# Kernel optimization log

Measured on AMD Instinct MI355X. Metric: run time of the kernel, lower is better.

Reference implementation:

```python
import jax, jax.numpy as jnp
import numpy as np

N_NODES = 100000
N_EDGES = 3200000
N_GRAPHS = 256
HID = 128


def _glorot(key, shape):
    fan_in = shape[1]
    return jax.random.normal(key, shape, dtype=jnp.float32) / jnp.sqrt(jnp.float32(fan_in))


def setup_inputs() -> dict:
    key = jax.random.key(0)
    ks = jax.random.split(key, 16)
    x = jax.random.normal(ks[0], (N_NODES, 50), dtype=jnp.float32)
    edge_index = jax.random.randint(ks[1], (2, N_EDGES), 0, N_NODES, dtype=jnp.int32)
    batch = jnp.sort(jax.random.randint(ks[2], (N_NODES,), 0, N_GRAPHS, dtype=jnp.int32))
    d1, d2, d3 = HID, HID * 2, HID * 4
    params = {
        'w1l': _glorot(ks[3], (d1, 50)), 'b1': jnp.zeros((d1,), jnp.float32), 'w1r': _glorot(ks[4], (d1, 50)),
        'w2l': _glorot(ks[5], (d2, d1)), 'b2': jnp.zeros((d2,), jnp.float32), 'w2r': _glorot(ks[6], (d2, d1)),
        'w3l': _glorot(ks[7], (d3, d2)), 'b3': jnp.zeros((d3,), jnp.float32), 'w3r': _glorot(ks[8], (d3, d2)),
        'fc1_w': _glorot(ks[9], (d2, d3)), 'fc1_b': jnp.zeros((d2,), jnp.float32),
        'fc2_w': _glorot(ks[10], (d1, d2)), 'fc2_b': jnp.zeros((d1,), jnp.float32),
        'cls_w': _glorot(ks[11], (15, d1)), 'cls_b': jnp.zeros((15,), jnp.float32),
    }
    return {'x': x, 'edge_index': edge_index, 'batch': batch, **params}


def _sage_conv(x, src, dst, wl, b, wr):
    # PyG SAGEConv (mean aggr): out = lin_l(mean_j x_j) + lin_r(x_i)
    agg = jax.ops.segment_sum(x[src], dst, num_segments=N_NODES)
    deg = jax.ops.segment_sum(jnp.ones((src.shape[0],), x.dtype), dst, num_segments=N_NODES)
    agg = agg / jnp.maximum(deg, 1.0)[:, None]
    return agg @ wl.T + b + x @ wr.T


def reference(x, edge_index, batch,
              w1l, b1, w1r, w2l, b2, w2r, w3l, b3, w3r,
              fc1_w, fc1_b, fc2_w, fc2_b, cls_w, cls_b):
    src, dst = edge_index[0], edge_index[1]
    # eval mode: dropout is identity
    h = jax.nn.leaky_relu(_sage_conv(x, src, dst, w1l, b1, w1r), negative_slope=0.01)
    h = jax.nn.relu(_sage_conv(h, src, dst, w2l, b2, w2r))
    h = jax.nn.relu(_sage_conv(h, src, dst, w3l, b3, w3r))
    # global mean pool over graphs
    pooled = jax.ops.segment_sum(h, batch, num_segments=N_GRAPHS)
    cnt = jax.ops.segment_sum(jnp.ones((h.shape[0],), h.dtype), batch, num_segments=N_GRAPHS)
    pooled = pooled / jnp.maximum(cnt, 1.0)[:, None]
    z = jax.nn.relu(pooled @ fc1_w.T + fc1_b)
    z = jax.nn.relu(z @ fc2_w.T + fc2_b)
    return z @ cls_w.T + cls_b
```

## Files before the change

### kernel.cpp

```cpp
#include <hip/hip_runtime.h>
#include <hip/hip_bf16.h>

#define N_NODES 100000
#define N_EDGES 3200000
#define N_GRAPHS 256
#define CAP 80
#define NB 1563
#define NPB 64
#define PBLK 512
#define EPB 6250

typedef __hip_bfloat16 bf16;
using f32x4  = __attribute__((ext_vector_type(4))) float;
using f32x2  = __attribute__((ext_vector_type(2))) float;
using short8 = __attribute__((ext_vector_type(8))) short;

__global__ __launch_bounds__(256) void p1_count(const int* __restrict__ dst,
                                                int* __restrict__ bcount) {
    __shared__ int hist[NB];
    int i = blockIdx.x;
    for (int b = threadIdx.x; b < NB; b += 256) hist[b] = 0;
    __syncthreads();
    int base = i * EPB;
    for (int j = threadIdx.x; j < EPB; j += 256)
        atomicAdd(&hist[dst[base + j] >> 6], 1);
    __syncthreads();
    for (int b = threadIdx.x; b < NB; b += 256) bcount[(size_t)b * PBLK + i] = hist[b];
}

__global__ __launch_bounds__(512) void p2a_total(const int* __restrict__ bcount,
                                                 int* __restrict__ btotal) {
    __shared__ int red[512];
    int b = blockIdx.x;
    red[threadIdx.x] = bcount[(size_t)b * PBLK + threadIdx.x];
    __syncthreads();
    for (int off = 256; off > 0; off >>= 1) {
        if (threadIdx.x < off) red[threadIdx.x] += red[threadIdx.x + off];
        __syncthreads();
    }
    if (threadIdx.x == 0) btotal[b] = red[0];
}

__global__ __launch_bounds__(1024) void p2b_scan(const int* __restrict__ btotal,
                                                 int* __restrict__ bbase) {
    __shared__ int buf[1024];
    __shared__ int carry;
    if (threadIdx.x == 0) carry = 0;
    __syncthreads();
    for (int t = 0; t < NB; t += 1024) {
        int i = t + threadIdx.x;
        int v = (i < NB) ? btotal[i] : 0;
        buf[threadIdx.x] = v;
        __syncthreads();
        for (int off = 1; off < 1024; off <<= 1) {
            int tv = (threadIdx.x >= off) ? buf[threadIdx.x - off] : 0;
            __syncthreads();
            buf[threadIdx.x] += tv;
            __syncthreads();
        }
        if (i < NB) bbase[i] = carry + buf[threadIdx.x] - v;
        __syncthreads();
        if (threadIdx.x == 0) carry += buf[1023];
        __syncthreads();
    }
    if (threadIdx.x == 0) bbase[NB] = carry;
}

__global__ __launch_bounds__(512) void p2c_off(const int* __restrict__ bcount,
                                               const int* __restrict__ bbase,
                                               int* __restrict__ off) {
    __shared__ int buf[512];
    int b = blockIdx.x;
    int v = bcount[(size_t)b * PBLK + threadIdx.x];
    buf[threadIdx.x] = v;
    __syncthreads();
    for (int o = 1; o < 512; o <<= 1) {
        int t = (threadIdx.x >= o) ? buf[threadIdx.x - o] : 0;
        __syncthreads();
        buf[threadIdx.x] += t;
        __syncthreads();
    }
    off[(size_t)threadIdx.x * NB + b] = bbase[b] + buf[threadIdx.x] - v;
}

__global__ __launch_bounds__(256) void p3_scatter(const int* __restrict__ src,
                                                  const int* __restrict__ dst,
                                                  const int* __restrict__ off,
                                                  unsigned int* __restrict__ ebuf) {
    __shared__ int loff[NB];
    int i = blockIdx.x;
    for (int b = threadIdx.x; b < NB; b += 256) loff[b] = off[(size_t)i * NB + b];
    __syncthreads();
    int base = i * EPB;
    for (int j = threadIdx.x; j < EPB; j += 256) {
        int d = dst[base + j];
        int p = atomicAdd(&loff[d >> 6], 1);
        ebuf[p] = ((unsigned)src[base + j] << 6) | (unsigned)(d & 63);
    }
}

__global__ __launch_bounds__(256) void p4_csr(const unsigned int* __restrict__ ebuf,
                                              const int* __restrict__ bbase,
                                              int* __restrict__ cols, int* __restrict__ cnt,
                                              float* __restrict__ invdeg) {
    __shared__ int lcnt[NPB];
    int b = blockIdx.x;
    if (threadIdx.x < NPB) lcnt[threadIdx.x] = 0;
    __syncthreads();
    int s = bbase[b], e = bbase[b + 1];
    int n0 = b * NPB;
    for (int j = s + threadIdx.x; j < e; j += 256) {
        unsigned int p = ebuf[j];
        int dl = p & 63;
        int r = atomicAdd(&lcnt[dl], 1);
        if (r < CAP) cols[(size_t)(n0 + dl) * CAP + r] = (int)(p >> 6);
    }
    __syncthreads();
    if (threadIdx.x < NPB) {
        int n = n0 + threadIdx.x;
        if (n < N_NODES) {
            int c = lcnt[threadIdx.x];
            cnt[n] = c;
            invdeg[n] = 1.0f / fmaxf((float)c, 1.0f);
        }
    }
}

__global__ void xprep_kernel(const float* __restrict__ x, unsigned char* __restrict__ xb8) {
    int t = blockIdx.x * blockDim.x + threadIdx.x;
    if (t >= N_NODES * 64) return;
    int n = t >> 6, f = t & 63;
    float v = (f < 50) ? x[(size_t)n * 50 + f] : 0.f;
    int p = __builtin_amdgcn_cvt_pk_fp8_f32(v, v, 0, false);
    xb8[t] = (unsigned char)(p & 0xff);
}

__device__ __forceinline__ void wcvt(const float* __restrict__ s, bf16* __restrict__ d,
                                     int Din, int Kp, int lt) {
    int o = lt / Kp, kk = lt % Kp;
    d[lt] = __float2bfloat16(kk < Din ? s[(size_t)o * Din + kk] : 0.f);
}

__global__ void wprep_all_kernel(const float* w1l, const float* w1r,
                                 const float* w2l, const float* w2r,
                                 const float* w3l, const float* w3r,
                                 bf16* w1l_b, bf16* w1r_b, bf16* w2l_b, bf16* w2r_b,
                                 bf16* w3l_b, bf16* w3r_b) {
    int t = blockIdx.x * blockDim.x + threadIdx.x;
    if      (t < 8192)   wcvt(w1l, w1l_b, 50, 64, t);
    else if (t < 16384)  wcvt(w1r, w1r_b, 50, 64, t - 8192);
    else if (t < 49152)  wcvt(w2l, w2l_b, 128, 128, t - 16384);
    else if (t < 81920)  wcvt(w2r, w2r_b, 128, 128, t - 49152);
    else if (t < 212992) wcvt(w3l, w3l_b, 256, 256, t - 81920);
    else if (t < 344064) wcvt(w3r, w3r_b, 256, 256, t - 212992);
}

template <int D>
__global__ void aggv8_kernel(const unsigned char* __restrict__ h8,
                             const int* __restrict__ cnt,
                             const int* __restrict__ cols, const float* __restrict__ invdeg,
                             unsigned char* __restrict__ AG8) {
    constexpr int L = D / 8;
    int n = blockIdx.x * (256 / L) + threadIdx.x / L;
    int lane = threadIdx.x % L;
    if (n >= N_NODES) return;
    const int* cp = cols + (size_t)n * CAP;
    int deg = min(cnt[n], CAP);
    float acc[8] = {};
    auto accum = [&](uint2 v) {
        f32x2 a0 = __builtin_amdgcn_cvt_pk_f32_fp8(v.x, false);
        f32x2 a1 = __builtin_amdgcn_cvt_pk_f32_fp8(v.x, true);
        f32x2 a2 = __builtin_amdgcn_cvt_pk_f32_fp8(v.y, false);
        f32x2 a3 = __builtin_amdgcn_cvt_pk_f32_fp8(v.y, true);
        acc[0] += a0[0]; acc[1] += a0[1]; acc[2] += a1[0]; acc[3] += a1[1];
        acc[4] += a2[0]; acc[5] += a2[1]; acc[6] += a3[0]; acc[7] += a3[1];
    };
    int j = 0;
    for (; j + 8 <= deg; j += 8) {
        uint2 v[8];
#pragma unroll
        for (int q = 0; q < 8; ++q)
            v[q] = *(const uint2*)&h8[(size_t)cp[j + q] * D + lane * 8];
#pragma unroll
        for (int q = 0; q < 8; ++q) accum(v[q]);
    }
    for (; j < deg; ++j) accum(*(const uint2*)&h8[(size_t)cp[j] * D + lane * 8]);
    float inv = invdeg[n];
    uint2 o;
    int w0 = __builtin_amdgcn_cvt_pk_fp8_f32(acc[0] * inv, acc[1] * inv, 0, false);
    w0     = __builtin_amdgcn_cvt_pk_fp8_f32(acc[2] * inv, acc[3] * inv, w0, true);
    int w1 = __builtin_amdgcn_cvt_pk_fp8_f32(acc[4] * inv, acc[5] * inv, 0, false);
    w1     = __builtin_amdgcn_cvt_pk_fp8_f32(acc[6] * inv, acc[7] * inv, w1, true);
    o.x = (unsigned)w0; o.y = (unsigned)w1;
    *(uint2*)&AG8[(size_t)n * D + lane * 8] = o;
}

__device__ __forceinline__ short8 cvt8(uint2 v) {
    f32x2 p0 = __builtin_amdgcn_cvt_pk_f32_fp8(v.x, false);
    f32x2 p1 = __builtin_amdgcn_cvt_pk_f32_fp8(v.x, true);
    f32x2 p2 = __builtin_amdgcn_cvt_pk_f32_fp8(v.y, false);
    f32x2 p3 = __builtin_amdgcn_cvt_pk_f32_fp8(v.y, true);
    union { short8 s; bf16 h[8]; } r;
    r.h[0] = __float2bfloat16(p0[0]); r.h[1] = __float2bfloat16(p0[1]);
    r.h[2] = __float2bfloat16(p1[0]); r.h[3] = __float2bfloat16(p1[1]);
    r.h[4] = __float2bfloat16(p2[0]); r.h[5] = __float2bfloat16(p2[1]);
    r.h[6] = __float2bfloat16(p3[0]); r.h[7] = __float2bfloat16(p3[1]);
    return r.s;
}

template <int ACT, int POOL, int NX>
__global__ __launch_bounds__(256) void fp8a_gemm(
        const unsigned char* __restrict__ A1, const unsigned char* __restrict__ A2, int Kh,
        const bf16* __restrict__ B1, const bf16* __restrict__ B2,
        const float* __restrict__ bias, unsigned char* __restrict__ out8,
        int M, int Dout,
        const int* __restrict__ batch, float* __restrict__ pooled) {
    __shared__ alignas(16) bf16 As[2][128][32];
    __shared__ alignas(16) bf16 Bs[2][128][32];
    __shared__ int sbatch[128];

    const int gid = blockIdx.x;
    const int group = gid / (8 * NX);
    const int rem = gid % (8 * NX);
    const int xcol = rem >> 3;
    const int ytile = group * 8 + (rem & 7);
    const int MBt = (M + 127) >> 7;
    if (ytile >= MBt) return;

    const int tid = threadIdx.x;
    const int n0 = ytile * 128;
    const int o0 = xcol * 128;

    if (POOL && tid < 128) {
        int n = n0 + tid;
        sbatch[tid] = (n < M) ? batch[n] : -1;
    }

    const int lane = tid & 63;
    const int w = tid >> 6;
    const int wr = w >> 1, wc = w & 1;
    const int lr = lane & 15, hi = lane >> 4;
    const int l4 = lane >> 2;
    const int kc8 = (lane & 3) * 8;

    f32x4 acc[4][4] = {};

    const int rl0 = w * 32 + l4;
    const int rl1 = rl0 + 16;

    auto issueA = [&](int k0, uint2& a0, uint2& a1v) {
        const unsigned char* Ap = (k0 < Kh) ? A1 : A2;
        int kk = (k0 < Kh) ? k0 : k0 - Kh;
        a0  = *(const uint2*)&Ap[(size_t)min(n0 + rl0, M - 1) * Kh + kk + kc8];
        a1v = *(const uint2*)&Ap[(size_t)min(n0 + rl1, M - 1) * Kh + kk + kc8];
    };
    auto issueB = [&](int buf, int k0) {
        const bf16* Bp = (k0 < Kh) ? B1 : B2;
        int kk = (k0 < Kh) ? k0 : k0 - Kh;
#pragma unroll
        for (int c = 0; c < 2; ++c) {
            int rl = w * 32 + c * 16 + l4;
            size_t gb = (size_t)(o0 + rl) * (size_t)Kh + kk + kc8;
            __builtin_amdgcn_global_load_lds(
                (const __attribute__((address_space(1))) void*)(Bp + gb),
                (__attribute__((address_space(3))) void*)&Bs[buf][w * 32 + c * 16][0], 16, 0, 0);
        }
    };
    auto writeA = [&](int buf, uint2 a0, uint2 a1v) {
        *(short8*)&As[buf][rl0][kc8] = cvt8(a0);
        *(short8*)&As[buf][rl1][kc8] = cvt8(a1v);
    };

    const int nt = (2 * Kh) / 32;
    uint2 ra0, ra1;
    issueA(0, ra0, ra1);
    issueB(0, 0);
    asm volatile("s_waitcnt vmcnt(0)" ::: "memory");
    writeA(0, ra0, ra1);
    __syncthreads();

    int cur = 0;
    for (int t = 0; t < nt; ++t) {
        if (t + 1 < nt) {
            issueA((t + 1) * 32, ra0, ra1);
            issueB(cur ^ 1, (t + 1) * 32);
        }

        short8 af[4], bfr[4];
#pragma unroll
        for (int m = 0; m < 4; ++m)
            af[m] = *(const short8*)&As[cur][wr * 64 + m * 16 + lr][hi * 8];
#pragma unroll
        for (int n = 0; n < 4; ++n)
            bfr[n] = *(const short8*)&Bs[cur][wc * 64 + n * 16 + lr][hi * 8];
#pragma unroll
        for (int m = 0; m < 4; ++m)
#pragma unroll
            for (int n = 0; n < 4; ++n)
                acc[m][n] = __builtin_amdgcn_mfma_f32_16x16x32_bf16(af[m], bfr[n], acc[m][n], 0, 0, 0);

        if (t + 1 < nt) {
            asm volatile("s_waitcnt vmcnt(0)" ::: "memory");
            writeA(cur ^ 1, ra0, ra1);
            __syncthreads();
        }
        cur ^= 1;
    }

    float bias_v[4];
#pragma unroll
    for (int n = 0; n < 4; ++n) bias_v[n] = bias[o0 + wc * 64 + n * 16 + lr];

    if (!POOL) {
#pragma unroll
        for (int m = 0; m < 4; ++m) {
#pragma unroll
            for (int j = 0; j < 4; ++j) {
                int row = n0 + wr * 64 + m * 16 + hi * 4 + j;
                if (row < M) {
#pragma unroll
                    for (int n = 0; n < 4; ++n) {
                        int col = o0 + wc * 64 + n * 16 + lr;
                        float s = acc[m][n][j] + bias_v[n];
                        if (ACT == 0) s = (s >= 0.f) ? s : 0.01f * s;
                        else          s = fmaxf(s, 0.f);
                        int p = __builtin_amdgcn_cvt_pk_fp8_f32(s, s, 0, false);
                        out8[(size_t)row * Dout + col] = (unsigned char)(p & 0xff);
                    }
                }
            }
        }
    } else {
        int lastv = min(127, M - 1 - n0);
        int gmin = sbatch[0], gmax = sbatch[lastv];
        for (int g = gmin; g <= gmax; ++g) {
            float s[4] = {0.f, 0.f, 0.f, 0.f};
#pragma unroll
            for (int m = 0; m < 4; ++m) {
#pragma unroll
                for (int j = 0; j < 4; ++j) {
                    int rl = wr * 64 + m * 16 + hi * 4 + j;
                    if (sbatch[rl] == g) {
#pragma unroll
                        for (int n = 0; n < 4; ++n)
                            s[n] += fmaxf(acc[m][n][j] + bias_v[n], 0.f);
                    }
                }
            }
#pragma unroll
            for (int n = 0; n < 4; ++n) {
                float v = s[n];
                v += __shfl_xor(v, 16, 64);
                v += __shfl_xor(v, 32, 64);
                if (hi == 0)
                    atomicAdd(&pooled[(size_t)g * 512 + o0 + wc * 64 + n * 16 + lr], v);
            }
        }
    }
}

__global__ void bounds_kernel(const int* __restrict__ batch, int* __restrict__ gstart) {
    int g = blockIdx.x * blockDim.x + threadIdx.x;
    if (g > N_GRAPHS) return;
    int lo = 0, hi = N_NODES;
    while (lo < hi) {
        int mid = (lo + hi) >> 1;
        if (batch[mid] < g) lo = mid + 1;
        else hi = mid;
    }
    gstart[g] = lo;
}

__global__ void pool_finalize(float* __restrict__ pooled, const int* __restrict__ gstart) {
    int g = blockIdx.x;
    int f = threadIdx.x;
    float cnt = fmaxf((float)(gstart[g + 1] - gstart[g]), 1.0f);
    pooled[(size_t)g * 512 + f] /= cnt;
}

template <int ACT>
__global__ void mlp_kernel(const float* __restrict__ in, const float* __restrict__ w,
                           const float* __restrict__ b, float* __restrict__ out,
                           int M, int K, int O) {
    int t = blockIdx.x * blockDim.x + threadIdx.x;
    if (t >= M * O) return;
    int m = t / O, o = t % O;
    const float* ip = in + (size_t)m * K;
    const float* wp = w + (size_t)o * K;
    float s = 0.f;
    for (int k = 0; k < K; ++k) s += ip[k] * wp[k];
    s += b[o];
    if (ACT) s = fmaxf(s, 0.f);
    out[(size_t)m * O + o] = s;
}

extern "C" void kernel_launch(void* const* d_in, const int* in_sizes, int n_in,
                              void* d_out, int out_size, void* d_ws, size_t ws_size,
                              hipStream_t stream) {
    const float* x     = (const float*)d_in[0];
    const int*   ei    = (const int*)d_in[1];
    const int*   batch = (const int*)d_in[2];
    const float* w1l = (const float*)d_in[3];
    const float* b1  = (const float*)d_in[4];
    const float* w1r = (const float*)d_in[5];
    const float* w2l = (const float*)d_in[6];
    const float* b2  = (const float*)d_in[7];
    const float* w2r = (const float*)d_in[8];
    const float* w3l = (const float*)d_in[9];
    const float* b3  = (const float*)d_in[10];
    const float* w3r = (const float*)d_in[11];
    const float* fc1_w = (const float*)d_in[12];
    const float* fc1_b = (const float*)d_in[13];
    const float* fc2_w = (const float*)d_in[14];
    const float* fc2_b = (const float*)d_in[15];
    const float* cls_w = (const float*)d_in[16];
    const float* cls_b = (const float*)d_in[17];
    float* out = (float*)d_out;

    const int* src = ei;
    const int* dst = ei + N_EDGES;

    char* wsp = (char*)d_ws;
    size_t used = 0;
    auto alloc = [&](size_t bytes) {
        char* p = wsp + used;
        used += (bytes + 255) & ~(size_t)255;
        return p;
    };
    int*   cnt    = (int*)alloc((size_t)N_NODES * 4);
    int*   cols   = (int*)alloc((size_t)N_NODES * CAP * 4);
    float* invdeg = (float*)alloc((size_t)N_NODES * 4);
    int*   gstart = (int*)alloc((size_t)(N_GRAPHS + 1) * 4);
    char*  xbdead = alloc((size_t)N_NODES * 64 * 2);
    char*  R      = alloc((size_t)N_NODES * 256 * 2);
    unsigned char* AG8 = (unsigned char*)R;
    char*  S51    = alloc((size_t)N_NODES * 256 * 2);
    unsigned char* h1_8 = (unsigned char*)alloc((size_t)N_NODES * 128);
    unsigned char* h2_8 = (unsigned char*)alloc((size_t)N_NODES * 256);
    bf16*  w1l_b  = (bf16*)alloc(128 * 64 * 2);
    bf16*  w1r_b  = (bf16*)alloc(128 * 64 * 2);
    bf16*  w2l_b  = (bf16*)alloc(256 * 128 * 2);
    bf16*  w2r_b  = (bf16*)alloc(256 * 128 * 2);
    bf16*  w3l_b  = (bf16*)alloc(512 * 256 * 2);
    bf16*  w3r_b  = (bf16*)alloc(512 * 256 * 2);
    float* pooled = (float*)alloc((size_t)N_GRAPHS * 512 * 4);
    float* z1     = (float*)alloc((size_t)N_GRAPHS * 256 * 4);
    float* z2     = (float*)alloc((size_t)N_GRAPHS * 128 * 4);
    (void)xbdead;

    int* bcount = (int*)(S51 + 16 * 1024 * 1024);
    int* btotal = bcount + (size_t)NB * PBLK;
    int* bbase  = btotal + NB;
    int* off    = bbase + NB + 1;
    unsigned int* ebuf = (unsigned int*)S51;
    unsigned char* xb8 = (unsigned char*)S51;

    if (ws_size < used) return;

    p1_count<<<PBLK, 256, 0, stream>>>(dst, bcount);
    p2a_total<<<NB, 512, 0, stream>>>(bcount, btotal);
    p2b_scan<<<1, 1024, 0, stream>>>(btotal, bbase);
    p2c_off<<<NB, 512, 0, stream>>>(bcount, bbase, off);
    p3_scatter<<<PBLK, 256, 0, stream>>>(src, dst, off, ebuf);
    p4_csr<<<NB, 256, 0, stream>>>(ebuf, bbase, cols, cnt, invdeg);
    bounds_kernel<<<2, 160, 0, stream>>>(batch, gstart);

    xprep_kernel<<<(N_NODES * 64 + 255) / 256, 256, 0, stream>>>(x, xb8);
    wprep_all_kernel<<<(344064 + 255) / 256, 256, 0, stream>>>(
        w1l, w1r, w2l, w2r, w3l, w3r, w1l_b, w1r_b, w2l_b, w2r_b, w3l_b, w3r_b);

    const int GB = 98 * 8;

    aggv8_kernel<64><<<(N_NODES * 8 + 255) / 256, 256, 0, stream>>>(
        xb8, cnt, cols, invdeg, AG8);
    fp8a_gemm<0, 0, 1><<<GB, 256, 0, stream>>>(
        AG8, xb8, 64, w1l_b, w1r_b, b1, h1_8, N_NODES, 128, nullptr, nullptr);

    aggv8_kernel<128><<<(N_NODES * 16 + 255) / 256, 256, 0, stream>>>(
        h1_8, cnt, cols, invdeg, AG8);
    fp8a_gemm<1, 0, 2><<<GB * 2, 256, 0, stream>>>(
        AG8, h1_8, 128, w2l_b, w2r_b, b2, h2_8, N_NODES, 256, nullptr, nullptr);

    aggv8_kernel<256><<<(N_NODES * 32 + 255) / 256, 256, 0, stream>>>(
        h2_8, cnt, cols, invdeg, AG8);
    hipMemsetAsync(pooled, 0, (size_t)N_GRAPHS * 512 * 4, stream);
    fp8a_gemm<1, 1, 4><<<GB * 4, 256, 0, stream>>>(
        AG8, h2_8, 256, w3l_b, w3r_b, b3, nullptr, N_NODES, 512, batch, pooled);
    pool_finalize<<<N_GRAPHS, 512, 0, stream>>>(pooled, gstart);

    mlp_kernel<1><<<(N_GRAPHS * 256 + 255) / 256, 256, 0, stream>>>(
        pooled, fc1_w, fc1_b, z1, N_GRAPHS, 512, 256);
    mlp_kernel<1><<<(N_GRAPHS * 128 + 255) / 256, 256, 0, stream>>>(
        z1, fc2_w, fc2_b, z2, N_GRAPHS, 256, 128);
    mlp_kernel<0><<<(N_GRAPHS * 15 + 255) / 256, 256, 0, stream>>>(
        z2, cls_w, cls_b, out, N_GRAPHS, 128, 15);
}
```

Before: 570.5 us.

## Switch GEMMs to native FP8 MFMA with hi/lo split FP8 weights

The GEMM kernels previously read FP8 activations, converted them to bf16 in registers and wrote them to LDS before running bf16 MFMA. Activations are now copied straight to LDS as FP8 with global_load_lds, and each weight is stored as a high FP8 part plus an FP8 residual, so fp8×fp8 MFMAs run twice per tile to keep weight precision. This removes the per-tile conversion work and the register-staged A path, and halves the LDS footprint of A. In exchange it doubles the MFMA count and adds the lo-weight loads, and accuracy relies on the residual split.

```diff
diff --git a/kernel.cpp b/kernel.cpp
--- a/kernel.cpp
+++ b/kernel.cpp
@@ -13,7 +13,6 @@
 typedef __hip_bfloat16 bf16;
 using f32x4  = __attribute__((ext_vector_type(4))) float;
 using f32x2  = __attribute__((ext_vector_type(2))) float;
-using short8 = __attribute__((ext_vector_type(8))) short;
 
 __global__ __launch_bounds__(256) void p1_count(const int* __restrict__ dst,
                                                 int* __restrict__ bcount) {
@@ -135,24 +134,32 @@
     xb8[t] = (unsigned char)(p & 0xff);
 }
 
-__device__ __forceinline__ void wcvt(const float* __restrict__ s, bf16* __restrict__ d,
-                                     int Din, int Kp, int lt) {
+__device__ __forceinline__ void wcvt2(const float* __restrict__ s, unsigned char* __restrict__ d,
+                                      int Din, int Kp, int Dout, int lt) {
     int o = lt / Kp, kk = lt % Kp;
-    d[lt] = __float2bfloat16(kk < Din ? s[(size_t)o * Din + kk] : 0.f);
+    float v = (kk < Din) ? s[(size_t)o * Din + kk] : 0.f;
+    int ph = __builtin_amdgcn_cvt_pk_fp8_f32(v, v, 0, false);
+    unsigned hb = (unsigned)(ph & 0xff);
+    f32x2 dec = __builtin_amdgcn_cvt_pk_f32_fp8(hb, false);
+    float r = v - dec[0];
+    int pl = __builtin_amdgcn_cvt_pk_fp8_f32(r, r, 0, false);
+    d[lt] = (unsigned char)hb;
+    d[(size_t)Dout * Kp + lt] = (unsigned char)(pl & 0xff);
 }
 
 __global__ void wprep_all_kernel(const float* w1l, const float* w1r,
                                  const float* w2l, const float* w2r,
                                  const float* w3l, const float* w3r,
-                                 bf16* w1l_b, bf16* w1r_b, bf16* w2l_b, bf16* w2r_b,
-                                 bf16* w3l_b, bf16* w3r_b) {
+                                 unsigned char* w1l_8, unsigned char* w1r_8,
+                                 unsigned char* w2l_8, unsigned char* w2r_8,
+                                 unsigned char* w3l_8, unsigned char* w3r_8) {
     int t = blockIdx.x * blockDim.x + threadIdx.x;
-    if      (t < 8192)   wcvt(w1l, w1l_b, 50, 64, t);
-    else if (t < 16384)  wcvt(w1r, w1r_b, 50, 64, t - 8192);
-    else if (t < 49152)  wcvt(w2l, w2l_b, 128, 128, t - 16384);
-    else if (t < 81920)  wcvt(w2r, w2r_b, 128, 128, t - 49152);
-    else if (t < 212992) wcvt(w3l, w3l_b, 256, 256, t - 81920);
-    else if (t < 344064) wcvt(w3r, w3r_b, 256, 256, t - 212992);
+    if      (t < 8192)   wcvt2(w1l, w1l_8, 50, 64, 128, t);
+    else if (t < 16384)  wcvt2(w1r, w1r_8, 50, 64, 128, t - 8192);
+    else if (t < 49152)  wcvt2(w2l, w2l_8, 128, 128, 256, t - 16384);
+    else if (t < 81920)  wcvt2(w2r, w2r_8, 128, 128, 256, t - 49152);
+    else if (t < 212992) wcvt2(w3l, w3l_8, 256, 256, 512, t - 81920);
+    else if (t < 344064) wcvt2(w3r, w3r_8, 256, 256, 512, t - 212992);
 }
 
 template <int D>
@@ -166,6 +173,7 @@
     if (n >= N_NODES) return;
     const int* cp = cols + (size_t)n * CAP;
     int deg = min(cnt[n], CAP);
+    const size_t fo = (size_t)lane * 8;
     float acc[8] = {};
     auto accum = [&](uint2 v) {
         f32x2 a0 = __builtin_amdgcn_cvt_pk_f32_fp8(v.x, false);
@@ -180,11 +188,11 @@
         uint2 v[8];
 #pragma unroll
         for (int q = 0; q < 8; ++q)
-            v[q] = *(const uint2*)&h8[(size_t)cp[j + q] * D + lane * 8];
+            v[q] = *(const uint2*)&h8[(size_t)cp[j + q] * D + fo];
 #pragma unroll
         for (int q = 0; q < 8; ++q) accum(v[q]);
     }
-    for (; j < deg; ++j) accum(*(const uint2*)&h8[(size_t)cp[j] * D + lane * 8]);
+    for (; j < deg; ++j) accum(*(const uint2*)&h8[(size_t)cp[j] * D + fo]);
     float inv = invdeg[n];
     uint2 o;
     int w0 = __builtin_amdgcn_cvt_pk_fp8_f32(acc[0] * inv, acc[1] * inv, 0, false);
@@ -192,31 +200,20 @@
     int w1 = __builtin_amdgcn_cvt_pk_fp8_f32(acc[4] * inv, acc[5] * inv, 0, false);
     w1     = __builtin_amdgcn_cvt_pk_fp8_f32(acc[6] * inv, acc[7] * inv, w1, true);
     o.x = (unsigned)w0; o.y = (unsigned)w1;
-    *(uint2*)&AG8[(size_t)n * D + lane * 8] = o;
-}
-
-__device__ __forceinline__ short8 cvt8(uint2 v) {
-    f32x2 p0 = __builtin_amdgcn_cvt_pk_f32_fp8(v.x, false);
-    f32x2 p1 = __builtin_amdgcn_cvt_pk_f32_fp8(v.x, true);
-    f32x2 p2 = __builtin_amdgcn_cvt_pk_f32_fp8(v.y, false);
-    f32x2 p3 = __builtin_amdgcn_cvt_pk_f32_fp8(v.y, true);
-    union { short8 s; bf16 h[8]; } r;
-    r.h[0] = __float2bfloat16(p0[0]); r.h[1] = __float2bfloat16(p0[1]);
-    r.h[2] = __float2bfloat16(p1[0]); r.h[3] = __float2bfloat16(p1[1]);
-    r.h[4] = __float2bfloat16(p2[0]); r.h[5] = __float2bfloat16(p2[1]);
-    r.h[6] = __float2bfloat16(p3[0]); r.h[7] = __float2bfloat16(p3[1]);
-    return r.s;
+    *(uint2*)&AG8[(size_t)n * D + fo] = o;
 }
 
 template <int ACT, int POOL, int NX>
-__global__ __launch_bounds__(256) void fp8a_gemm(
+__global__ __launch_bounds__(256) void fp8_gemm(
         const unsigned char* __restrict__ A1, const unsigned char* __restrict__ A2, int Kh,
-        const bf16* __restrict__ B1, const bf16* __restrict__ B2,
+        const unsigned char* __restrict__ B1h, const unsigned char* __restrict__ B1l,
+        const unsigned char* __restrict__ B2h, const unsigned char* __restrict__ B2l,
         const float* __restrict__ bias, unsigned char* __restrict__ out8,
         int M, int Dout,
         const int* __restrict__ batch, float* __restrict__ pooled) {
-    __shared__ alignas(16) bf16 As[2][128][32];
-    __shared__ alignas(16) bf16 Bs[2][128][32];
+    __shared__ alignas(16) unsigned char As[2][128][32];
+    __shared__ alignas(16) unsigned char Bsh[2][128][32];
+    __shared__ alignas(16) unsigned char Bsl[2][128][32];
     __shared__ int sbatch[128];
 
     const int gid = blockIdx.x;
@@ -240,70 +237,55 @@
     const int w = tid >> 6;
     const int wr = w >> 1, wc = w & 1;
     const int lr = lane & 15, hi = lane >> 4;
-    const int l4 = lane >> 2;
-    const int kc8 = (lane & 3) * 8;
+    const int srow = w * 32 + (lane >> 1);
+    const int scol = (lane & 1) * 16;
 
     f32x4 acc[4][4] = {};
 
-    const int rl0 = w * 32 + l4;
-    const int rl1 = rl0 + 16;
-
-    auto issueA = [&](int k0, uint2& a0, uint2& a1v) {
+    auto stage = [&](int buf, int k0) {
         const unsigned char* Ap = (k0 < Kh) ? A1 : A2;
+        const unsigned char* Bph = (k0 < Kh) ? B1h : B2h;
+        const unsigned char* Bpl = (k0 < Kh) ? B1l : B2l;
         int kk = (k0 < Kh) ? k0 : k0 - Kh;
-        a0  = *(const uint2*)&Ap[(size_t)min(n0 + rl0, M - 1) * Kh + kk + kc8];
-        a1v = *(const uint2*)&Ap[(size_t)min(n0 + rl1, M - 1) * Kh + kk + kc8];
+        size_t ga = (size_t)min(n0 + srow, M - 1) * (size_t)Kh + kk + scol;
+        __builtin_amdgcn_global_load_lds(
+            (const __attribute__((address_space(1))) void*)(Ap + ga),
+            (__attribute__((address_space(3))) void*)&As[buf][w * 32][0], 16, 0, 0);
+        size_t gb = (size_t)(o0 + srow) * (size_t)Kh + kk + scol;
+        __builtin_amdgcn_global_load_lds(
+            (const __attribute__((address_space(1))) void*)(Bph + gb),
+            (__attribute__((address_space(3))) void*)&Bsh[buf][w * 32][0], 16, 0, 0);
+        __builtin_amdgcn_global_load_lds(
+            (const __attribute__((address_space(1))) void*)(Bpl + gb),
+            (__attribute__((address_space(3))) void*)&Bsl[buf][w * 32][0], 16, 0, 0);
     };
-    auto issueB = [&](int buf, int k0) {
-        const bf16* Bp = (k0 < Kh) ? B1 : B2;
-        int kk = (k0 < Kh) ? k0 : k0 - Kh;
-#pragma unroll
-        for (int c = 0; c < 2; ++c) {
-            int rl = w * 32 + c * 16 + l4;
-            size_t gb = (size_t)(o0 + rl) * (size_t)Kh + kk + kc8;
-            __builtin_amdgcn_global_load_lds(
-                (const __attribute__((address_space(1))) void*)(Bp + gb),
-                (__attribute__((address_space(3))) void*)&Bs[buf][w * 32 + c * 16][0], 16, 0, 0);
-        }
-    };
-    auto writeA = [&](int buf, uint2 a0, uint2 a1v) {
-        *(short8*)&As[buf][rl0][kc8] = cvt8(a0);
-        *(short8*)&As[buf][rl1][kc8] = cvt8(a1v);
-    };
 
     const int nt = (2 * Kh) / 32;
-    uint2 ra0, ra1;
-    issueA(0, ra0, ra1);
-    issueB(0, 0);
-    asm volatile("s_waitcnt vmcnt(0)" ::: "memory");
-    writeA(0, ra0, ra1);
+    stage(0, 0);
     __syncthreads();
 
     int cur = 0;
     for (int t = 0; t < nt; ++t) {
-        if (t + 1 < nt) {
-            issueA((t + 1) * 32, ra0, ra1);
-            issueB(cur ^ 1, (t + 1) * 32);
+        if (t + 1 < nt) stage(cur ^ 1, (t + 1) * 32);
+
+        long af[4], bh[4], bl[4];
+#pragma unroll
+        for (int m = 0; m < 4; ++m)
+            af[m] = *(const long*)&As[cur][wr * 64 + m * 16 + lr][hi * 8];
+#pragma unroll
+        for (int n = 0; n < 4; ++n) {
+            bh[n] = *(const long*)&Bsh[cur][wc * 64 + n * 16 + lr][hi * 8];
+            bl[n] = *(const long*)&Bsl[cur][wc * 64 + n * 16 + lr][hi * 8];
         }
-
-        short8 af[4], bfr[4];
 #pragma unroll
         for (int m = 0; m < 4; ++m)
-            af[m] = *(const short8*)&As[cur][wr * 64 + m * 16 + lr][hi * 8];
-#pragma unroll
-        for (int n = 0; n < 4; ++n)
-            bfr[n] = *(const short8*)&Bs[cur][wc * 64 + n * 16 + lr][hi * 8];
-#pragma unroll
-        for (int m = 0; m < 4; ++m)
-#pragma unroll
-            for (int n = 0; n < 4; ++n)
-                acc[m][n] = __builtin_amdgcn_mfma_f32_16x16x32_bf16(af[m], bfr[n], acc[m][n], 0, 0, 0);
-
-        if (t + 1 < nt) {
-            asm volatile("s_waitcnt vmcnt(0)" ::: "memory");
-            writeA(cur ^ 1, ra0, ra1);
-            __syncthreads();
-        }
+#pragma unroll
+            for (int n = 0; n < 4; ++n) {
+                acc[m][n] = __builtin_amdgcn_mfma_f32_16x16x32_fp8_fp8(af[m], bh[n], acc[m][n], 0, 0, 0);
+                acc[m][n] = __builtin_amdgcn_mfma_f32_16x16x32_fp8_fp8(af[m], bl[n], acc[m][n], 0, 0, 0);
+            }
+
+        __syncthreads();
         cur ^= 1;
     }
 
@@ -437,12 +419,12 @@
     char*  S51    = alloc((size_t)N_NODES * 256 * 2);
     unsigned char* h1_8 = (unsigned char*)alloc((size_t)N_NODES * 128);
     unsigned char* h2_8 = (unsigned char*)alloc((size_t)N_NODES * 256);
-    bf16*  w1l_b  = (bf16*)alloc(128 * 64 * 2);
-    bf16*  w1r_b  = (bf16*)alloc(128 * 64 * 2);
-    bf16*  w2l_b  = (bf16*)alloc(256 * 128 * 2);
-    bf16*  w2r_b  = (bf16*)alloc(256 * 128 * 2);
-    bf16*  w3l_b  = (bf16*)alloc(512 * 256 * 2);
-    bf16*  w3r_b  = (bf16*)alloc(512 * 256 * 2);
+    unsigned char* w1l_8 = (unsigned char*)alloc(128 * 64 * 2);
+    unsigned char* w1r_8 = (unsigned char*)alloc(128 * 64 * 2);
+    unsigned char* w2l_8 = (unsigned char*)alloc(256 * 128 * 2);
+    unsigned char* w2r_8 = (unsigned char*)alloc(256 * 128 * 2);
+    unsigned char* w3l_8 = (unsigned char*)alloc(512 * 256 * 2);
+    unsigned char* w3r_8 = (unsigned char*)alloc(512 * 256 * 2);
     float* pooled = (float*)alloc((size_t)N_GRAPHS * 512 * 4);
     float* z1     = (float*)alloc((size_t)N_GRAPHS * 256 * 4);
     float* z2     = (float*)alloc((size_t)N_GRAPHS * 128 * 4);
@@ -467,25 +449,31 @@
 
     xprep_kernel<<<(N_NODES * 64 + 255) / 256, 256, 0, stream>>>(x, xb8);
     wprep_all_kernel<<<(344064 + 255) / 256, 256, 0, stream>>>(
-        w1l, w1r, w2l, w2r, w3l, w3r, w1l_b, w1r_b, w2l_b, w2r_b, w3l_b, w3r_b);
+        w1l, w1r, w2l, w2r, w3l, w3r, w1l_8, w1r_8, w2l_8, w2r_8, w3l_8, w3r_8);
 
     const int GB = 98 * 8;
 
     aggv8_kernel<64><<<(N_NODES * 8 + 255) / 256, 256, 0, stream>>>(
         xb8, cnt, cols, invdeg, AG8);
-    fp8a_gemm<0, 0, 1><<<GB, 256, 0, stream>>>(
-        AG8, xb8, 64, w1l_b, w1r_b, b1, h1_8, N_NODES, 128, nullptr, nullptr);
+    fp8_gemm<0, 0, 1><<<GB, 256, 0, stream>>>(
+        AG8, xb8, 64,
+        w1l_8, w1l_8 + 128 * 64, w1r_8, w1r_8 + 128 * 64,
+        b1, h1_8, N_NODES, 128, nullptr, nullptr);
 
     aggv8_kernel<128><<<(N_NODES * 16 + 255) / 256, 256, 0, stream>>>(
         h1_8, cnt, cols, invdeg, AG8);
-    fp8a_gemm<1, 0, 2><<<GB * 2, 256, 0, stream>>>(
-        AG8, h1_8, 128, w2l_b, w2r_b, b2, h2_8, N_NODES, 256, nullptr, nullptr);
+    fp8_gemm<1, 0, 2><<<GB * 2, 256, 0, stream>>>(
+        AG8, h1_8, 128,
+        w2l_8, w2l_8 + 256 * 128, w2r_8, w2r_8 + 256 * 128,
+        b2, h2_8, N_NODES, 256, nullptr, nullptr);
 
     aggv8_kernel<256><<<(N_NODES * 32 + 255) / 256, 256, 0, stream>>>(
         h2_8, cnt, cols, invdeg, AG8);
     hipMemsetAsync(pooled, 0, (size_t)N_GRAPHS * 512 * 4, stream);
-    fp8a_gemm<1, 1, 4><<<GB * 4, 256, 0, stream>>>(
-        AG8, h2_8, 256, w3l_b, w3r_b, b3, nullptr, N_NODES, 512, batch, pooled);
+    fp8_gemm<1, 1, 4><<<GB * 4, 256, 0, stream>>>(
+        AG8, h2_8, 256,
+        w3l_8, w3l_8 + 512 * 256, w3r_8, w3r_8 + 512 * 256,
+        b3, nullptr, N_NODES, 512, batch, pooled);
     pool_finalize<<<N_GRAPHS, 512, 0, stream>>>(pooled, gstart);
 
     mlp_kernel<1><<<(N_GRAPHS * 256 + 255) / 256, 256, 0, stream>>>(
```

Result: slower. 597.0 us (+4.6%).

## Stage fp8 A tiles directly into LDS and convert at fragment load

Applied to the files above, without the earlier changes.

The GEMM now loads the fp8 A operand straight into LDS with asynchronous global_load_lds, the same way B is loaded, instead of going through registers, converting to bf16 and then writing to LDS. The fp8-to-bf16 conversion moves to the point where each wave reads its MFMA fragments. XOR swizzles are added to the staging and read column indices to reduce LDS bank conflicts. This removes the explicit vmcnt wait and register round-trip in the pipeline and halves A's LDS footprint, at the cost of repeating the conversion per wave (each A fragment is converted by both column waves) and an unconditional barrier every iteration.

```diff
diff --git a/kernel.cpp b/kernel.cpp
--- a/kernel.cpp
+++ b/kernel.cpp
@@ -166,6 +166,7 @@
     if (n >= N_NODES) return;
     const int* cp = cols + (size_t)n * CAP;
     int deg = min(cnt[n], CAP);
+    const size_t fo = (size_t)lane * 8;
     float acc[8] = {};
     auto accum = [&](uint2 v) {
         f32x2 a0 = __builtin_amdgcn_cvt_pk_f32_fp8(v.x, false);
@@ -180,11 +181,11 @@
         uint2 v[8];
 #pragma unroll
         for (int q = 0; q < 8; ++q)
-            v[q] = *(const uint2*)&h8[(size_t)cp[j + q] * D + lane * 8];
+            v[q] = *(const uint2*)&h8[(size_t)cp[j + q] * D + fo];
 #pragma unroll
         for (int q = 0; q < 8; ++q) accum(v[q]);
     }
-    for (; j < deg; ++j) accum(*(const uint2*)&h8[(size_t)cp[j] * D + lane * 8]);
+    for (; j < deg; ++j) accum(*(const uint2*)&h8[(size_t)cp[j] * D + fo]);
     float inv = invdeg[n];
     uint2 o;
     int w0 = __builtin_amdgcn_cvt_pk_fp8_f32(acc[0] * inv, acc[1] * inv, 0, false);
@@ -192,7 +193,7 @@
     int w1 = __builtin_amdgcn_cvt_pk_fp8_f32(acc[4] * inv, acc[5] * inv, 0, false);
     w1     = __builtin_amdgcn_cvt_pk_fp8_f32(acc[6] * inv, acc[7] * inv, w1, true);
     o.x = (unsigned)w0; o.y = (unsigned)w1;
-    *(uint2*)&AG8[(size_t)n * D + lane * 8] = o;
+    *(uint2*)&AG8[(size_t)n * D + fo] = o;
 }
 
 __device__ __forceinline__ short8 cvt8(uint2 v) {
@@ -209,13 +210,13 @@
 }
 
 template <int ACT, int POOL, int NX>
-__global__ __launch_bounds__(256) void fp8a_gemm(
+__global__ __launch_bounds__(256) void hyb_gemm(
         const unsigned char* __restrict__ A1, const unsigned char* __restrict__ A2, int Kh,
         const bf16* __restrict__ B1, const bf16* __restrict__ B2,
         const float* __restrict__ bias, unsigned char* __restrict__ out8,
         int M, int Dout,
         const int* __restrict__ batch, float* __restrict__ pooled) {
-    __shared__ alignas(16) bf16 As[2][128][32];
+    __shared__ alignas(16) unsigned char As[2][128][32];
     __shared__ alignas(16) bf16 Bs[2][128][32];
     __shared__ int sbatch[128];
 
@@ -240,70 +241,58 @@
     const int w = tid >> 6;
     const int wr = w >> 1, wc = w & 1;
     const int lr = lane & 15, hi = lane >> 4;
-    const int l4 = lane >> 2;
-    const int kc8 = (lane & 3) * 8;
+
+    const int srowA = w * 32 + (lane >> 1);
+    const int scolA = ((lane & 1) ^ ((lane >> 3) & 1)) * 16;
+    const int srowB_l = lane >> 2;
+    const int scolB = ((lane & 3) ^ ((lane >> 3) & 3)) * 8;
+    const int rcolA = (hi ^ (((lr >> 2) & 1) << 1)) * 8;
+    const int rcolB = (hi ^ ((lr >> 1) & 3)) * 8;
 
     f32x4 acc[4][4] = {};
 
-    const int rl0 = w * 32 + l4;
-    const int rl1 = rl0 + 16;
-
-    auto issueA = [&](int k0, uint2& a0, uint2& a1v) {
+    auto stage = [&](int buf, int k0) {
         const unsigned char* Ap = (k0 < Kh) ? A1 : A2;
-        int kk = (k0 < Kh) ? k0 : k0 - Kh;
-        a0  = *(const uint2*)&Ap[(size_t)min(n0 + rl0, M - 1) * Kh + kk + kc8];
-        a1v = *(const uint2*)&Ap[(size_t)min(n0 + rl1, M - 1) * Kh + kk + kc8];
-    };
-    auto issueB = [&](int buf, int k0) {
         const bf16* Bp = (k0 < Kh) ? B1 : B2;
         int kk = (k0 < Kh) ? k0 : k0 - Kh;
+        size_t ga = (size_t)min(n0 + srowA, M - 1) * (size_t)Kh + kk + scolA;
+        __builtin_amdgcn_global_load_lds(
+            (const __attribute__((address_space(1))) void*)(Ap + ga),
+            (__attribute__((address_space(3))) void*)&As[buf][w * 32][0], 16, 0, 0);
 #pragma unroll
         for (int c = 0; c < 2; ++c) {
-            int rl = w * 32 + c * 16 + l4;
-            size_t gb = (size_t)(o0 + rl) * (size_t)Kh + kk + kc8;
+            int row = w * 32 + c * 16 + srowB_l;
+            size_t gb = (size_t)(o0 + row) * (size_t)Kh + kk + scolB;
             __builtin_amdgcn_global_load_lds(
                 (const __attribute__((address_space(1))) void*)(Bp + gb),
                 (__attribute__((address_space(3))) void*)&Bs[buf][w * 32 + c * 16][0], 16, 0, 0);
         }
     };
-    auto writeA = [&](int buf, uint2 a0, uint2 a1v) {
-        *(short8*)&As[buf][rl0][kc8] = cvt8(a0);
-        *(short8*)&As[buf][rl1][kc8] = cvt8(a1v);
-    };
 
     const int nt = (2 * Kh) / 32;
-    uint2 ra0, ra1;
-    issueA(0, ra0, ra1);
-    issueB(0, 0);
-    asm volatile("s_waitcnt vmcnt(0)" ::: "memory");
-    writeA(0, ra0, ra1);
+    stage(0, 0);
     __syncthreads();
 
     int cur = 0;
     for (int t = 0; t < nt; ++t) {
-        if (t + 1 < nt) {
-            issueA((t + 1) * 32, ra0, ra1);
-            issueB(cur ^ 1, (t + 1) * 32);
-        }
+        if (t + 1 < nt) stage(cur ^ 1, (t + 1) * 32);
 
         short8 af[4], bfr[4];
 #pragma unroll
-        for (int m = 0; m < 4; ++m)
-            af[m] = *(const short8*)&As[cur][wr * 64 + m * 16 + lr][hi * 8];
+        for (int m = 0; m < 4; ++m) {
+            uint2 a8 = *(const uint2*)&As[cur][wr * 64 + m * 16 + lr][rcolA];
+            af[m] = cvt8(a8);
+        }
 #pragma unroll
         for (int n = 0; n < 4; ++n)
-            bfr[n] = *(const short8*)&Bs[cur][wc * 64 + n * 16 + lr][hi * 8];
+            bfr[n] = *(const short8*)&Bs[cur][wc * 64 + n * 16 + lr][rcolB];
 #pragma unroll
         for (int m = 0; m < 4; ++m)
 #pragma unroll
             for (int n = 0; n < 4; ++n)
                 acc[m][n] = __builtin_amdgcn_mfma_f32_16x16x32_bf16(af[m], bfr[n], acc[m][n], 0, 0, 0);
 
-        if (t + 1 < nt) {
-            asm volatile("s_waitcnt vmcnt(0)" ::: "memory");
-            writeA(cur ^ 1, ra0, ra1);
-            __syncthreads();
-        }
+        __syncthreads();
         cur ^= 1;
     }
 
@@ -473,18 +462,18 @@
 
     aggv8_kernel<64><<<(N_NODES * 8 + 255) / 256, 256, 0, stream>>>(
         xb8, cnt, cols, invdeg, AG8);
-    fp8a_gemm<0, 0, 1><<<GB, 256, 0, stream>>>(
+    hyb_gemm<0, 0, 1><<<GB, 256, 0, stream>>>(
         AG8, xb8, 64, w1l_b, w1r_b, b1, h1_8, N_NODES, 128, nullptr, nullptr);
 
     aggv8_kernel<128><<<(N_NODES * 16 + 255) / 256, 256, 0, stream>>>(
         h1_8, cnt, cols, invdeg, AG8);
-    fp8a_gemm<1, 0, 2><<<GB * 2, 256, 0, stream>>>(
+    hyb_gemm<1, 0, 2><<<GB * 2, 256, 0, stream>>>(
         AG8, h1_8, 128, w2l_b, w2r_b, b2, h2_8, N_NODES, 256, nullptr, nullptr);
 
     aggv8_kernel<256><<<(N_NODES * 32 + 255) / 256, 256, 0, stream>>>(
         h2_8, cnt, cols, invdeg, AG8);
     hipMemsetAsync(pooled, 0, (size_t)N_GRAPHS * 512 * 4, stream);
-    fp8a_gemm<1, 1, 4><<<GB * 4, 256, 0, stream>>>(
+    hyb_gemm<1, 1, 4><<<GB * 4, 256, 0, stream>>>(
         AG8, h2_8, 256, w3l_b, w3r_b, b3, nullptr, N_NODES, 512, batch, pooled);
     pool_finalize<<<N_GRAPHS, 512, 0, stream>>>(pooled, gstart);
 
```

New measurement: 563.0 us. Within noise of the previous version (-1.3%).
